# Kernel tuning notes

Measured on AMD Instinct MI355X. Metric: run time of the kernel, lower is better.

## Reference

```python
import jax, jax.numpy as jnp
import numpy as np

B, N, C = 4096, 49, 256       # windows, tokens-per-window (7*7), channels
H, HD = 8, 32                 # heads, head_dim
WIN = 7                       # window side
M = 64                        # mask_shape (num windows per image)
SCALE = HD ** -0.5


def _relative_position_index():
    coords = np.stack(np.meshgrid(np.arange(WIN), np.arange(WIN), indexing='ij'))
    flat = coords.reshape(2, -1)                      # [2, 49]
    rel = flat[:, :, None] - flat[:, None, :]         # [2, 49, 49]
    rel = rel.transpose(1, 2, 0).astype(np.int32)     # [49, 49, 2]
    rel[:, :, 0] += WIN - 1
    rel[:, :, 1] += WIN - 1
    rel[:, :, 0] *= 2 * WIN - 1
    return rel.sum(-1)                                # [49, 49], values in [0, 169)


def setup_inputs() -> dict:
    key = jax.random.key(0)
    k1, k2, k3, k4, k5 = jax.random.split(key, 5)
    hidden_states = jax.random.normal(k1, (B, N, C), dtype=jnp.float32)
    attention_mask = jax.random.normal(k2, (M, N, N), dtype=jnp.float32)
    qkv_w = jax.random.normal(k3, (3 * C, C), dtype=jnp.float32) * 0.02
    qkv_b = jax.random.normal(k4, (3 * C,), dtype=jnp.float32) * 0.02
    bias_table = jax.random.normal(k5, ((2 * WIN - 1) ** 2, H), dtype=jnp.float32) * 0.02
    rel_index = jnp.asarray(_relative_position_index())
    return {"hidden_states": hidden_states, "attention_mask": attention_mask,
            "qkv_w": qkv_w, "qkv_b": qkv_b, "bias_table": bias_table,
            "rel_index": rel_index}


def reference(hidden_states, attention_mask, qkv_w, qkv_b, bias_table, rel_index):
    b, n, c = hidden_states.shape
    qkv = hidden_states @ qkv_w.T + qkv_b            # [B, N, 3C]
    q, k, v = jnp.split(qkv, 3, axis=-1)
    to_heads = lambda x: x.reshape(b, n, H, HD).transpose(0, 2, 1, 3)  # [B,H,N,HD]
    q, k, v = to_heads(q), to_heads(k), to_heads(v)

    # relative position bias: gather table -> [N, N, H] -> [H, N, N]
    bias = bias_table[rel_index.reshape(-1)].reshape(n, n, H).transpose(2, 0, 1)

    # mask[j] is applied to window-batch index b where j = b mod M
    m = attention_mask.shape[0]
    full = bias[None, None] + attention_mask[None, :, None]   # [1, M, H, N, N]
    full = jnp.broadcast_to(full, (b // m, m, H, n, n)).reshape(b, H, n, n)

    scores = jnp.einsum('bhqd,bhkd->bhqk', q, k) * SCALE + full
    attn = jax.nn.softmax(scores, axis=-1)
    ctx = jnp.einsum('bhqk,bhkd->bhqd', attn, v)
    return ctx.transpose(0, 2, 1, 3).reshape(b, n, c)
```

## Files before the change

### kernel.cpp

```cpp
#include <hip/hip_runtime.h>
#include <hip/hip_bf16.h>
#include <stdint.h>

typedef unsigned short u16;
typedef __attribute__((ext_vector_type(8))) short bf16x8;
typedef __attribute__((ext_vector_type(8))) unsigned short u16x8;
typedef __attribute__((ext_vector_type(4))) float f32x4;

#define NTOK 49
#define CDIM 256
#define NHEAD 8
#define HDIM 32
#define SCALE_F 0.17677669529663687f

static __device__ inline u16 f2b(float f) {
    union { float f; unsigned u; } v; v.f = f;
    unsigned r = v.u + 0x7fff + ((v.u >> 16) & 1);
    return (u16)(r >> 16);
}

#define GLOAD_LDS16(g, l) __builtin_amdgcn_global_load_lds( \
    (const __attribute__((address_space(1))) unsigned int*)(g), \
    (__attribute__((address_space(3))) unsigned int*)(l), 16, 0, 0)

__global__ __launch_bounds__(256) void conv_bf16(
    const float* __restrict__ src, u16* __restrict__ dst, int n8)
{
    int i = blockIdx.x * 256 + threadIdx.x;
    if (i < n8) {
        float4 a = ((const float4*)src)[2 * i];
        float4 b = ((const float4*)src)[2 * i + 1];
        u16x8 v;
        v[0] = f2b(a.x); v[1] = f2b(a.y); v[2] = f2b(a.z); v[3] = f2b(a.w);
        v[4] = f2b(b.x); v[5] = f2b(b.y); v[6] = f2b(b.z); v[7] = f2b(b.w);
        ((u16x8*)dst)[i] = v;
    }
}

__global__ __launch_bounds__(256) void build_comb(
    const float* __restrict__ bias_table,
    const float* __restrict__ mask,
    const int*   __restrict__ rel_index,
    float* __restrict__ comb)
{
    int idx = blockIdx.x * 256 + threadIdx.x;
    int j = idx & 63, i = (idx >> 6) & 63, h = (idx >> 12) & 7, m = idx >> 15;
    float v = -1e9f;
    if (i < NTOK && j < NTOK) {
        int rel = rel_index[i * NTOK + j];
        v = bias_table[rel * NHEAD + h] + mask[m * (NTOK * NTOK) + i * NTOK + j];
    }
    comb[idx] = v;
}

__global__ __launch_bounds__(256) void qkv_gemm(
    const u16*  __restrict__ A,
    const u16*  __restrict__ Wt,
    const float* __restrict__ bias,
    u16* __restrict__ Cout)
{
    __shared__ u16 As[128 * 64];
    __shared__ u16 Bs[128 * 64];

    const int t = threadIdx.x;
    const int bm = blockIdx.x, bn = blockIdx.y;
    const int wave = t >> 6, lane = t & 63;
    const int wm = wave >> 1, wn = wave & 1;
    const int lrow = lane & 15, quad = lane >> 4;

    f32x4 acc[4][4];
#pragma unroll
    for (int i = 0; i < 4; i++)
#pragma unroll
        for (int j = 0; j < 4; j++) acc[i][j] = (f32x4){0.f, 0.f, 0.f, 0.f};

    const int dr = lane >> 3;
    const int dc = ((lane & 7) ^ dr) * 8;
    const u16* Ag = A  + (size_t)(bm * 128 + wave * 32) * CDIM;
    const u16* Bg = Wt + (size_t)(bn * 128 + wave * 32) * CDIM;

#pragma unroll
    for (int kt = 0; kt < 4; kt++) {
        if (kt) __syncthreads();
        const int k0 = kt * 64;
#pragma unroll
        for (int i = 0; i < 4; i++) {
            GLOAD_LDS16(Ag + (size_t)(i * 8 + dr) * CDIM + k0 + dc, &As[(wave * 32 + i * 8) * 64]);
            GLOAD_LDS16(Bg + (size_t)(i * 8 + dr) * CDIM + k0 + dc, &Bs[(wave * 32 + i * 8) * 64]);
        }
        __syncthreads();
#pragma unroll
        for (int kk = 0; kk < 2; kk++) {
            const int xr = kk * 4 + quad;
            const int sw = ((xr ^ (lrow & 7)) << 3);
            bf16x8 af[4], bfr[4];
#pragma unroll
            for (int tm = 0; tm < 4; tm++)
                af[tm] = *(const bf16x8*)&As[(wm * 64 + tm * 16 + lrow) * 64 + sw];
#pragma unroll
            for (int tn = 0; tn < 4; tn++)
                bfr[tn] = *(const bf16x8*)&Bs[(wn * 64 + tn * 16 + lrow) * 64 + sw];
#pragma unroll
            for (int tm = 0; tm < 4; tm++)
#pragma unroll
                for (int tn = 0; tn < 4; tn++)
                    acc[tm][tn] = __builtin_amdgcn_mfma_f32_16x16x32_bf16(
                        af[tm], bfr[tn], acc[tm][tn], 0, 0, 0);
        }
    }

#pragma unroll
    for (int tn = 0; tn < 4; tn++) {
        int gcol = bn * 128 + wn * 64 + tn * 16 + lrow;
        float bv = bias[gcol];
#pragma unroll
        for (int tm = 0; tm < 4; tm++) {
            int grow0 = bm * 128 + wm * 64 + tm * 16 + quad * 4;
#pragma unroll
            for (int r = 0; r < 4; r++)
                Cout[(size_t)(grow0 + r) * 768 + gcol] = f2b(acc[tm][tn][r] + bv);
        }
    }
}

__global__ __launch_bounds__(64, 2) void win_attn(
    const u16*   __restrict__ qkv,
    const float* __restrict__ comb,
    float* __restrict__ out,
    int G4)
{
    __shared__ u16 vT[32 * 72];
    __shared__ u16 P[64 * 72];

    const int lane = threadIdx.x, lrow = lane & 15, quad = lane >> 4;
    const int m = blockIdx.x;
    const int h = blockIdx.y / G4;
    const int grp = blockIdx.y % G4;
    const int qo = h * HDIM, ko = CDIM + h * HDIM, vo = 2 * CDIM + h * HDIM;

    f32x4 cmb[4][4];
    const float* cb = comb + (((size_t)m * NHEAD + h) << 12);
#pragma unroll
    for (int tm = 0; tm < 4; tm++)
#pragma unroll
        for (int r = 0; r < 4; r++) {
            const float* crow = cb + (tm * 16 + quad * 4 + r) * 64 + lrow;
#pragma unroll
            for (int tn = 0; tn < 4; tn++) cmb[tm][tn][r] = crow[tn * 16];
        }

    for (int c = lane; c < 32 * 15; c += 64) vT[(c / 15) * 72 + NTOK + (c % 15)] = 0;

    for (int j = 0; j < 4; j++) {
        const int lw = m + 64 * (grp * 4 + j);
        const size_t rb = (size_t)lw * NTOK * 768;

        for (int c = lane; c < NTOK * 8; c += 64) {
            int tok = c >> 3, d0 = (c & 7) * 4;
            uint2 v = *(const uint2*)&qkv[rb + (size_t)tok * 768 + vo + d0];
            vT[(d0 + 0) * 72 + tok] = (u16)(v.x & 0xffff);
            vT[(d0 + 1) * 72 + tok] = (u16)(v.x >> 16);
            vT[(d0 + 2) * 72 + tok] = (u16)(v.y & 0xffff);
            vT[(d0 + 3) * 72 + tok] = (u16)(v.y >> 16);
        }

        bf16x8 af[4], bfr[4];
#pragma unroll
        for (int tm = 0; tm < 4; tm++)
            af[tm]  = *(const bf16x8*)&qkv[rb + (size_t)(tm * 16 + lrow) * 768 + qo + quad * 8];
#pragma unroll
        for (int tn = 0; tn < 4; tn++)
            bfr[tn] = *(const bf16x8*)&qkv[rb + (size_t)(tn * 16 + lrow) * 768 + ko + quad * 8];

        f32x4 s[4][4];
#pragma unroll
        for (int a = 0; a < 4; a++)
#pragma unroll
            for (int b = 0; b < 4; b++) s[a][b] = (f32x4){0.f, 0.f, 0.f, 0.f};
#pragma unroll
        for (int tm = 0; tm < 4; tm++)
#pragma unroll
            for (int tn = 0; tn < 4; tn++)
                s[tm][tn] = __builtin_amdgcn_mfma_f32_16x16x32_bf16(af[tm], bfr[tn], s[tm][tn], 0, 0, 0);

#pragma unroll
        for (int tm = 0; tm < 4; tm++)
#pragma unroll
            for (int tn = 0; tn < 4; tn++)
#pragma unroll
                for (int r = 0; r < 4; r++)
                    s[tm][tn][r] = s[tm][tn][r] * SCALE_F + cmb[tm][tn][r];

#pragma unroll
        for (int tm = 0; tm < 4; tm++)
#pragma unroll
            for (int r = 0; r < 4; r++) {
                float e0 = __expf(s[tm][0][r]);
                float e1 = __expf(s[tm][1][r]);
                float e2 = __expf(s[tm][2][r]);
                float e3 = __expf(s[tm][3][r]);
                float sum = e0 + e1 + e2 + e3;
                sum += __shfl_xor(sum, 1);
                sum += __shfl_xor(sum, 2);
                sum += __shfl_xor(sum, 4);
                sum += __shfl_xor(sum, 8);
                float inv = 1.0f / sum;
                int i = tm * 16 + quad * 4 + r;
                P[i * 72 + lrow]      = f2b(e0 * inv);
                P[i * 72 + 16 + lrow] = f2b(e1 * inv);
                P[i * 72 + 32 + lrow] = f2b(e2 * inv);
                P[i * 72 + 48 + lrow] = f2b(e3 * inv);
            }

        f32x4 o[4][2];
#pragma unroll
        for (int a = 0; a < 4; a++) { o[a][0] = (f32x4){0.f,0.f,0.f,0.f}; o[a][1] = (f32x4){0.f,0.f,0.f,0.f}; }
#pragma unroll
        for (int kk = 0; kk < 2; kk++) {
            const int kb = kk * 32 + quad * 8;
            bf16x8 pf[4], vf[2];
#pragma unroll
            for (int tm = 0; tm < 4; tm++) pf[tm] = *(const bf16x8*)&P[(tm * 16 + lrow) * 72 + kb];
#pragma unroll
            for (int tn = 0; tn < 2; tn++) vf[tn] = *(const bf16x8*)&vT[(tn * 16 + lrow) * 72 + kb];
#pragma unroll
            for (int tm = 0; tm < 4; tm++)
#pragma unroll
                for (int tn = 0; tn < 2; tn++)
                    o[tm][tn] = __builtin_amdgcn_mfma_f32_16x16x32_bf16(pf[tm], vf[tn], o[tm][tn], 0, 0, 0);
        }

        float* ob = out + (size_t)lw * NTOK * CDIM + h * HDIM;
#pragma unroll
        for (int tm = 0; tm < 4; tm++)
#pragma unroll
            for (int r = 0; r < 4; r++) {
                int i = tm * 16 + quad * 4 + r;
                if (i < NTOK) {
                    ob[(size_t)i * CDIM + lrow]      = o[tm][0][r];
                    ob[(size_t)i * CDIM + 16 + lrow] = o[tm][1][r];
                }
            }
    }
}

extern "C" void kernel_launch(void* const* d_in, const int* in_sizes, int n_in,
                              void* d_out, int out_size, void* d_ws, size_t ws_size,
                              hipStream_t stream) {
    const float* hidden     = (const float*)d_in[0];
    const float* mask       = (const float*)d_in[1];
    const float* qkv_w      = (const float*)d_in[2];
    const float* qkv_b      = (const float*)d_in[3];
    const float* bias_table = (const float*)d_in[4];
    const int*   rel_index  = (const int*)d_in[5];
    float* out = (float*)d_out;

    float* comb = (float*)d_ws;
    u16* wbuf = (u16*)((char*)d_ws + 8388608);
    int W = 4096;
    while (W > 256 &&
           8388608ull + 393216ull + (size_t)W * NTOK * CDIM * 2
                      + (size_t)W * NTOK * 768 * 2 + 65536ull > ws_size)
        W >>= 1;
    const int nch = 4096 / W;
    const int G4 = W / 256;
    u16* hbuf = wbuf + 196608;
    u16* qkvbuf = hbuf + (size_t)W * NTOK * CDIM;

    build_comb<<<dim3(8192), dim3(256), 0, stream>>>(bias_table, mask, rel_index, comb);
    conv_bf16<<<dim3(96), dim3(256), 0, stream>>>(qkv_w, wbuf, 196608 / 8);

    const int ce = W * NTOK * CDIM;
    for (int c = 0; c < nch; c++) {
        conv_bf16<<<dim3((ce / 8 + 255) / 256), dim3(256), 0, stream>>>(
            hidden + (size_t)c * ce, hbuf, ce / 8);
        qkv_gemm<<<dim3(W * NTOK / 128, 6), dim3(256), 0, stream>>>(
            hbuf, wbuf, qkv_b, qkvbuf);
        win_attn<<<dim3(64, NHEAD * G4), dim3(64), 0, stream>>>(
            qkvbuf, comb, out + (size_t)c * ce, G4);
    }
}
```

Before: 679.9 us.

## Keep attention probabilities in registers via transposed S=K·Qᵀ and deferred normalization

Result: slower. 727.3 us (+7.0%).

```diff
diff --git a/kernel.cpp b/kernel.cpp
--- a/kernel.cpp
+++ b/kernel.cpp
@@ -4,6 +4,7 @@
 
 typedef unsigned short u16;
 typedef __attribute__((ext_vector_type(8))) short bf16x8;
+typedef __attribute__((ext_vector_type(4))) short bf16x4;
 typedef __attribute__((ext_vector_type(8))) unsigned short u16x8;
 typedef __attribute__((ext_vector_type(4))) float f32x4;
 
@@ -123,14 +124,13 @@
     }
 }
 
-__global__ __launch_bounds__(64, 2) void win_attn(
+__global__ __launch_bounds__(64, 4) void win_attn(
     const u16*   __restrict__ qkv,
     const float* __restrict__ comb,
     float* __restrict__ out,
     int G4)
 {
     __shared__ u16 vT[32 * 72];
-    __shared__ u16 P[64 * 72];
 
     const int lane = threadIdx.x, lrow = lane & 15, quad = lane >> 4;
     const int m = blockIdx.x;
@@ -138,16 +138,7 @@
     const int grp = blockIdx.y % G4;
     const int qo = h * HDIM, ko = CDIM + h * HDIM, vo = 2 * CDIM + h * HDIM;
 
-    f32x4 cmb[4][4];
     const float* cb = comb + (((size_t)m * NHEAD + h) << 12);
-#pragma unroll
-    for (int tm = 0; tm < 4; tm++)
-#pragma unroll
-        for (int r = 0; r < 4; r++) {
-            const float* crow = cb + (tm * 16 + quad * 4 + r) * 64 + lrow;
-#pragma unroll
-            for (int tn = 0; tn < 4; tn++) cmb[tm][tn][r] = crow[tn * 16];
-        }
 
     for (int c = lane; c < 32 * 15; c += 64) vT[(c / 15) * 72 + NTOK + (c % 15)] = 0;
 
@@ -164,83 +155,99 @@
             vT[(d0 + 3) * 72 + tok] = (u16)(v.y >> 16);
         }
 
-        bf16x8 af[4], bfr[4];
-#pragma unroll
-        for (int tm = 0; tm < 4; tm++)
-            af[tm]  = *(const bf16x8*)&qkv[rb + (size_t)(tm * 16 + lrow) * 768 + qo + quad * 8];
+        bf16x8 bq[4];
 #pragma unroll
         for (int tn = 0; tn < 4; tn++)
-            bfr[tn] = *(const bf16x8*)&qkv[rb + (size_t)(tn * 16 + lrow) * 768 + ko + quad * 8];
-
-        f32x4 s[4][4];
-#pragma unroll
-        for (int a = 0; a < 4; a++)
-#pragma unroll
-            for (int b = 0; b < 4; b++) s[a][b] = (f32x4){0.f, 0.f, 0.f, 0.f};
-#pragma unroll
-        for (int tm = 0; tm < 4; tm++)
-#pragma unroll
-            for (int tn = 0; tn < 4; tn++)
-                s[tm][tn] = __builtin_amdgcn_mfma_f32_16x16x32_bf16(af[tm], bfr[tn], s[tm][tn], 0, 0, 0);
-
-#pragma unroll
-        for (int tm = 0; tm < 4; tm++)
-#pragma unroll
-            for (int tn = 0; tn < 4; tn++)
-#pragma unroll
-                for (int r = 0; r < 4; r++)
-                    s[tm][tn][r] = s[tm][tn][r] * SCALE_F + cmb[tm][tn][r];
-
-#pragma unroll
-        for (int tm = 0; tm < 4; tm++)
-#pragma unroll
-            for (int r = 0; r < 4; r++) {
-                float e0 = __expf(s[tm][0][r]);
-                float e1 = __expf(s[tm][1][r]);
-                float e2 = __expf(s[tm][2][r]);
-                float e3 = __expf(s[tm][3][r]);
-                float sum = e0 + e1 + e2 + e3;
-                sum += __shfl_xor(sum, 1);
-                sum += __shfl_xor(sum, 2);
-                sum += __shfl_xor(sum, 4);
-                sum += __shfl_xor(sum, 8);
-                float inv = 1.0f / sum;
-                int i = tm * 16 + quad * 4 + r;
-                P[i * 72 + lrow]      = f2b(e0 * inv);
-                P[i * 72 + 16 + lrow] = f2b(e1 * inv);
-                P[i * 72 + 32 + lrow] = f2b(e2 * inv);
-                P[i * 72 + 48 + lrow] = f2b(e3 * inv);
-            }
-
-        f32x4 o[4][2];
-#pragma unroll
-        for (int a = 0; a < 4; a++) { o[a][0] = (f32x4){0.f,0.f,0.f,0.f}; o[a][1] = (f32x4){0.f,0.f,0.f,0.f}; }
-#pragma unroll
-        for (int kk = 0; kk < 2; kk++) {
-            const int kb = kk * 32 + quad * 8;
-            bf16x8 pf[4], vf[2];
-#pragma unroll
-            for (int tm = 0; tm < 4; tm++) pf[tm] = *(const bf16x8*)&P[(tm * 16 + lrow) * 72 + kb];
-#pragma unroll
-            for (int tn = 0; tn < 2; tn++) vf[tn] = *(const bf16x8*)&vT[(tn * 16 + lrow) * 72 + kb];
-#pragma unroll
-            for (int tm = 0; tm < 4; tm++)
-#pragma unroll
-                for (int tn = 0; tn < 2; tn++)
-                    o[tm][tn] = __builtin_amdgcn_mfma_f32_16x16x32_bf16(pf[tm], vf[tn], o[tm][tn], 0, 0, 0);
-        }
-
-        float* ob = out + (size_t)lw * NTOK * CDIM + h * HDIM;
-#pragma unroll
-        for (int tm = 0; tm < 4; tm++)
-#pragma unroll
-            for (int r = 0; r < 4; r++) {
-                int i = tm * 16 + quad * 4 + r;
-                if (i < NTOK) {
-                    ob[(size_t)i * CDIM + lrow]      = o[tm][0][r];
-                    ob[(size_t)i * CDIM + 16 + lrow] = o[tm][1][r];
+            bq[tn] = *(const bf16x8*)&qkv[rb + (size_t)(tn * 16 + lrow) * 768 + qo + quad * 8];
+
+        float sum[4] = {0.f, 0.f, 0.f, 0.f};
+        bf16x4 pk[4][4];
+
+#pragma unroll
+        for (int half = 0; half < 2; half++) {
+            bf16x8 ak[2];
+#pragma unroll
+            for (int t = 0; t < 2; t++)
+                ak[t] = *(const bf16x8*)&qkv[rb + (size_t)((half * 2 + t) * 16 + lrow) * 768 + ko + quad * 8];
+            f32x4 s[2][4];
+#pragma unroll
+            for (int t = 0; t < 2; t++)
+#pragma unroll
+                for (int tn = 0; tn < 4; tn++) s[t][tn] = (f32x4){0.f, 0.f, 0.f, 0.f};
+#pragma unroll
+            for (int t = 0; t < 2; t++)
+#pragma unroll
+                for (int tn = 0; tn < 4; tn++)
+                    s[t][tn] = __builtin_amdgcn_mfma_f32_16x16x32_bf16(ak[t], bq[tn], s[t][tn], 0, 0, 0);
+
+#pragma unroll
+            for (int t = 0; t < 2; t++) {
+                const int kt = half * 2 + t;
+#pragma unroll
+                for (int tn = 0; tn < 4; tn++) {
+                    float4 cv = *(const float4*)&cb[(size_t)(tn * 16 + lrow) * 64 + kt * 16 + quad * 4];
+                    float e0 = __expf(s[t][tn][0] * SCALE_F + cv.x);
+                    float e1 = __expf(s[t][tn][1] * SCALE_F + cv.y);
+                    float e2 = __expf(s[t][tn][2] * SCALE_F + cv.z);
+                    float e3 = __expf(s[t][tn][3] * SCALE_F + cv.w);
+                    sum[tn] += (e0 + e1) + (e2 + e3);
+                    bf16x4 p;
+                    p[0] = (short)f2b(e0); p[1] = (short)f2b(e1);
+                    p[2] = (short)f2b(e2); p[3] = (short)f2b(e3);
+                    pk[kt][tn] = p;
                 }
             }
+        }
+
+        float inv[4];
+#pragma unroll
+        for (int tn = 0; tn < 4; tn++) {
+            float sm = sum[tn];
+            sm += __shfl_xor(sm, 16);
+            sm += __shfl_xor(sm, 32);
+            inv[tn] = 1.0f / sm;
+        }
+
+        f32x4 o[2][4];
+#pragma unroll
+        for (int td = 0; td < 2; td++)
+#pragma unroll
+            for (int tn = 0; tn < 4; tn++) o[td][tn] = (f32x4){0.f, 0.f, 0.f, 0.f};
+#pragma unroll
+        for (int kt = 0; kt < 4; kt++) {
+            bf16x4 va[2];
+#pragma unroll
+            for (int td = 0; td < 2; td++)
+                va[td] = *(const bf16x4*)&vT[(td * 16 + lrow) * 72 + kt * 16 + quad * 4];
+#pragma unroll
+            for (int td = 0; td < 2; td++)
+#pragma unroll
+                for (int tn = 0; tn < 4; tn++)
+#if __has_builtin(__builtin_amdgcn_mfma_f32_16x16x16bf16_1k)
+                    o[td][tn] = __builtin_amdgcn_mfma_f32_16x16x16bf16_1k(
+                        va[td], pk[kt][tn], o[td][tn], 0, 0, 0);
+#else
+                    asm volatile("v_mfma_f32_16x16x16_bf16 %0, %1, %2, %0"
+                                 : "+v"(o[td][tn]) : "v"(va[td]), "v"(pk[kt][tn]));
+#endif
+        }
+
+        float* ob = out + (size_t)lw * NTOK * CDIM + h * HDIM;
+#pragma unroll
+        for (int tn = 0; tn < 4; tn++) {
+            int q = tn * 16 + lrow;
+            if (q < NTOK) {
+#pragma unroll
+                for (int td = 0; td < 2; td++) {
+                    float4 st;
+                    st.x = o[td][tn][0] * inv[tn];
+                    st.y = o[td][tn][1] * inv[tn];
+                    st.z = o[td][tn][2] * inv[tn];
+                    st.w = o[td][tn][3] * inv[tn];
+                    *(float4*)&ob[(size_t)q * CDIM + td * 16 + quad * 4] = st;
+                }
+            }
+        }
     }
 }
 
```
